# Kernel tuning notes

Measured on AMD Instinct MI355X. Metric: run time of the kernel, lower is better.

## Reference

```python
import jax, jax.numpy as jnp
import numpy as np


def setup_inputs() -> dict:
    key = jax.random.key(0)
    ks = jax.random.split(key, 10)
    B, N, F, H = 4, 512, 64, 4
    x = jax.random.normal(ks[0], (B, N, F), dtype=jnp.float32)
    adj = jax.random.uniform(ks[1], (N, N), dtype=jnp.float32)
    s = 1.0 / np.sqrt(F)
    Wq = jax.random.normal(ks[2], (F, F * H), dtype=jnp.float32) * s
    bq = jnp.zeros((F * H,), dtype=jnp.float32)
    Wk = jax.random.normal(ks[3], (F, F * H), dtype=jnp.float32) * s
    bk = jnp.zeros((F * H,), dtype=jnp.float32)
    Wlin = jax.random.normal(ks[4], (H, F), dtype=jnp.float32) * (1.0 / np.sqrt(H))
    blin = jnp.zeros((F,), dtype=jnp.float32)
    Wfc = jax.random.normal(ks[5], (F, F), dtype=jnp.float32) * s
    bfc = jnp.zeros((F,), dtype=jnp.float32)
    return {"x": x, "adj": adj, "Wq": Wq, "bq": bq, "Wk": Wk, "bk": bk,
            "Wlin": Wlin, "blin": blin, "Wfc": Wfc, "bfc": bfc}


def reference(x, adj, Wq, bq, Wk, bk, Wlin, blin, Wfc, bfc):
    B, N, F = x.shape
    H = Wlin.shape[0]
    # multi-head attention matrix (value projection is computed but unused in the original)
    q = (x @ Wq + bq).reshape(B, N, H, F)  # [B,N,H,F]
    k = (x @ Wk + bk).reshape(B, N, H, F)
    scores = jnp.einsum('bihf,bjhf->bhij', q, k) / jnp.sqrt(jnp.float32(F))
    attn = jax.nn.softmax(scores, axis=-1)  # [B,H,N,N]
    # linear over heads: [B,N,N,H] @ [H,F] -> [B,N,N,F]
    SV2 = jnp.einsum('bhij,hf->bijf', attn, Wlin) + blin
    # symmetric normalization of (adj + I)
    A = adj + jnp.eye(N, dtype=adj.dtype)
    d = jnp.sum(A, axis=1) ** -0.5
    noradj = d[:, None] * A * d[None, :]  # [N,N]
    # sum over dim 1 (source index i) of noradj[i,j]*SV2[b,i,j,f]*x[b,j,f]
    S = jnp.einsum('ij,bijf->bjf', noradj, SV2)
    sx = x * S  # [B,N,F]
    out = jnp.einsum('ij,bjf->bif', noradj, sx)
    out = out @ Wfc + bfc
    return jax.nn.relu(out)
```

## Files before the change

### kernel.cpp

```cpp
#include <hip/hip_runtime.h>
#include <math.h>

#define NN 512
#define FF 64
#define HH 4


__global__ __launch_bounds__(256) void k_s1(const float* __restrict__ x,
                                            const float* __restrict__ Wq,
                                            const float* __restrict__ bq,
                                            const float* __restrict__ Wk,
                                            const float* __restrict__ bk,
                                            const float* __restrict__ adj,
                                            float* __restrict__ q_t,
                                            float* __restrict__ kT,
                                            float* __restrict__ dinv,
                                            float* __restrict__ T,
                                            float* __restrict__ cvec) {
    __shared__ float x_lds[4][64];
    int blk = blockIdx.x, tid = threadIdx.x;
    int wave = tid >> 6, lane = tid & 63;

    if (blk < 512 && wave == 0) {
        float acc = 0.f;
#pragma unroll
        for (int k = 0; k < 8; ++k) acc += adj[(long)blk * NN + k * 64 + lane];
        for (int o = 32; o > 0; o >>= 1) acc += __shfl_xor(acc, o);
        if (lane == 0) dinv[blk] = 1.0f / sqrtf(acc + 1.0f);
    }
    if (blk < 128 && wave == 1) T[blk * 64 + lane] = 0.f;
    if (blk < 8 && wave == 2) cvec[blk * 64 + lane] = 0.f;

    int b = blk >> 8, rest = blk & 255, isK = rest >> 7, itile = rest & 127;
    int i0 = itile * 4;
    x_lds[tid >> 6][tid & 63] = x[((long)b * NN + i0 + (tid >> 6)) * FF + (tid & 63)];
    __syncthreads();
    const float* W = isK ? Wk : Wq;
    float bv = (isK ? bk : bq)[tid];
    float a0 = bv, a1 = bv, a2 = bv, a3 = bv;
    for (int cc = 0; cc < 64; ++cc) {
        float w = W[cc * 256 + tid];
        a0 = fmaf(x_lds[0][cc], w, a0);
        a1 = fmaf(x_lds[1][cc], w, a1);
        a2 = fmaf(x_lds[2][cc], w, a2);
        a3 = fmaf(x_lds[3][cc], w, a3);
    }
    int h = tid >> 6, f = tid & 63;
    int bh = b * HH + h;
    if (!isK) {
        long base = ((long)bh * NN + i0) * FF + f;
        q_t[base] = a0; q_t[base + FF] = a1;
        q_t[base + 2 * FF] = a2; q_t[base + 3 * FF] = a3;
    } else {
        float* kp = kT + (((long)(bh * 16 + (f >> 2)) * NN + i0) << 2) + (f & 3);
        kp[0] = a0; kp[4] = a1; kp[8] = a2; kp[12] = a3;
    }
}

__global__ __launch_bounds__(256) void k_s2(const float* __restrict__ q_t,
                                            const float* __restrict__ kT,
                                            const float* __restrict__ adj,
                                            const float* __restrict__ dinv,
                                            float* __restrict__ T,
                                            float* __restrict__ cvec) {
    __shared__ float q_lds[8][64];
    __shared__ float red[8][4];
    __shared__ float red2[8][4];
    int blk = blockIdx.x, tid = threadIdx.x;
    int itile = blk & 63, h = (blk >> 6) & 3, b = blk >> 8;
    int bh = b * HH + h, i0 = itile * 8;
    int wv = tid >> 6, lane = tid & 63;
#pragma unroll
    for (int k = 0; k < 2; ++k) {
        int idx = k * 256 + tid;
        q_lds[idx >> 6][idx & 63] =
            q_t[((long)bh * NN + i0 + (idx >> 6)) * FF + (idx & 63)];
    }
    __syncthreads();
    int j0 = tid, j1 = tid + 256;
    const float4* kb4 = (const float4*)kT + (long)bh * 16 * NN;
    float s0[8], s1[8];
#pragma unroll
    for (int r = 0; r < 8; ++r) { s0[r] = 0.f; s1[r] = 0.f; }
#pragma unroll 4
    for (int g = 0; g < 16; ++g) {
        float4 kv0 = kb4[g * NN + j0];
        float4 kv1 = kb4[g * NN + j1];
#pragma unroll
        for (int r = 0; r < 8; ++r) {
            float4 qv = *(const float4*)&q_lds[r][g * 4];
            s0[r] = fmaf(qv.x, kv0.x, s0[r]);
            s0[r] = fmaf(qv.y, kv0.y, s0[r]);
            s0[r] = fmaf(qv.z, kv0.z, s0[r]);
            s0[r] = fmaf(qv.w, kv0.w, s0[r]);
            s1[r] = fmaf(qv.x, kv1.x, s1[r]);
            s1[r] = fmaf(qv.y, kv1.y, s1[r]);
            s1[r] = fmaf(qv.z, kv1.z, s1[r]);
            s1[r] = fmaf(qv.w, kv1.w, s1[r]);
        }
    }
    const float scale = 0.125f;
    float m[8];
#pragma unroll
    for (int r = 0; r < 8; ++r) {
        float v = fmaxf(s0[r], s1[r]);
        for (int o = 32; o > 0; o >>= 1) v = fmaxf(v, __shfl_xor(v, o));
        if (lane == 0) red[r][wv] = v;
    }
    __syncthreads();
#pragma unroll
    for (int r = 0; r < 8; ++r)
        m[r] = fmaxf(fmaxf(red[r][0], red[r][1]), fmaxf(red[r][2], red[r][3]));
#pragma unroll
    for (int r = 0; r < 8; ++r) {
        s0[r] = __expf((s0[r] - m[r]) * scale);
        s1[r] = __expf((s1[r] - m[r]) * scale);
        float v = s0[r] + s1[r];
        for (int o = 32; o > 0; o >>= 1) v += __shfl_xor(v, o);
        if (lane == 0) red2[r][wv] = v;
    }
    __syncthreads();
    float dj0 = dinv[j0], dj1 = dinv[j1];
    float pw0 = 0.f, pw1 = 0.f, cw0 = 0.f, cw1 = 0.f;
#pragma unroll
    for (int r = 0; r < 8; ++r) {
        float Zi = 1.0f / (red2[r][0] + red2[r][1] + red2[r][2] + red2[r][3]);
        int gi = i0 + r;
        float di = dinv[gi];
        float a0 = adj[(long)gi * NN + j0] + (gi == j0 ? 1.f : 0.f);
        float a1 = adj[(long)gi * NN + j1] + (gi == j1 ? 1.f : 0.f);
        float t0 = di * a0, t1 = di * a1;
        pw0 = fmaf(t0, s0[r] * Zi, pw0);
        pw1 = fmaf(t1, s1[r] * Zi, pw1);
        cw0 += t0;
        cw1 += t1;
    }
    atomicAdd(&T[bh * NN + j0], pw0 * dj0);
    atomicAdd(&T[bh * NN + j1], pw1 * dj1);
    if (b == 0 && h == 0) {
        atomicAdd(&cvec[j0], cw0);
        atomicAdd(&cvec[j1], cw1);
    }
}

__global__ __launch_bounds__(256) void k_s3(const float* __restrict__ x,
                                            const float* __restrict__ T,
                                            const float* __restrict__ Wlin,
                                            const float* __restrict__ blin,
                                            const float* __restrict__ cvec,
                                            const float* __restrict__ adj,
                                            const float* __restrict__ dinv,
                                            const float* __restrict__ Wfc,
                                            const float* __restrict__ bfc,
                                            float* __restrict__ out) {
    __shared__ float4 u4_l[NN];
    __shared__ float  u0_l[NN];
    __shared__ float2 ad_l[NN];
    __shared__ float part[4][2][64];
    __shared__ float m_lds[2][64];
    __shared__ float part2[4][2][64];
    int blk = blockIdx.x, tid = threadIdx.x;
    int b = blk >> 8, itile = blk & 255;
    int i0 = itile * 2;

    for (int jj = tid; jj < NN; jj += 256) {
        float dj = dinv[jj];
        u0_l[jj] = dj * dj * cvec[jj];
        u4_l[jj] = make_float4(dj * T[(b * HH + 0) * NN + jj],
                               dj * T[(b * HH + 1) * NN + jj],
                               dj * T[(b * HH + 2) * NN + jj],
                               dj * T[(b * HH + 3) * NN + jj]);
        ad_l[jj] = make_float2(adj[(long)i0 * NN + jj] + (i0 == jj ? 1.f : 0.f),
                               adj[(long)(i0 + 1) * NN + jj] + (i0 + 1 == jj ? 1.f : 0.f));
    }
    __syncthreads();

    int f = tid & 63, jc = tid >> 6;
    int jb = jc * 128;
    float blf = blin[f];
    float4 wl = make_float4(Wlin[f], Wlin[64 + f], Wlin[128 + f], Wlin[192 + f]);
    const float* xb = x + (long)b * NN * FF + f;
    float a0 = 0.f, a1 = 0.f;
#pragma unroll 4
    for (int j = jb; j < jb + 128; ++j) {
        float xv = xb[(long)j * FF];
        float4 u = u4_l[j];
        float2 ad = ad_l[j];
        float S = blf * u0_l[j];
        S = fmaf(wl.x, u.x, S);
        S = fmaf(wl.y, u.y, S);
        S = fmaf(wl.z, u.z, S);
        S = fmaf(wl.w, u.w, S);
        float sx = xv * S;
        a0 = fmaf(ad.x, sx, a0);
        a1 = fmaf(ad.y, sx, a1);
    }
    part[jc][0][f] = a0;
    part[jc][1][f] = a1;
    __syncthreads();
    if (jc == 0) {
        m_lds[0][f] = (part[0][0][f] + part[1][0][f] + part[2][0][f] + part[3][0][f]) * dinv[i0];
        m_lds[1][f] = (part[0][1][f] + part[1][1][f] + part[2][1][f] + part[3][1][f]) * dinv[i0 + 1];
    }
    __syncthreads();
    float o0 = 0.f, o1 = 0.f;
    int c0 = jc * 16;
#pragma unroll
    for (int cc = 0; cc < 16; ++cc) {
        float w = Wfc[(c0 + cc) * FF + f];
        o0 = fmaf(m_lds[0][c0 + cc], w, o0);
        o1 = fmaf(m_lds[1][c0 + cc], w, o1);
    }
    part2[jc][0][f] = o0;
    part2[jc][1][f] = o1;
    __syncthreads();
    if (jc == 0) {
        float bb = bfc[f];
        float r0 = part2[0][0][f] + part2[1][0][f] + part2[2][0][f] + part2[3][0][f] + bb;
        float r1 = part2[0][1][f] + part2[1][1][f] + part2[2][1][f] + part2[3][1][f] + bb;
        out[((long)b * NN + i0) * FF + f]     = fmaxf(r0, 0.f);
        out[((long)b * NN + i0 + 1) * FF + f] = fmaxf(r1, 0.f);
    }
}

extern "C" void kernel_launch(void* const* d_in, const int* in_sizes, int n_in,
                              void* d_out, int out_size, void* d_ws, size_t ws_size,
                              hipStream_t stream) {
    const float* x    = (const float*)d_in[0];
    const float* adj  = (const float*)d_in[1];
    const float* Wq   = (const float*)d_in[2];
    const float* bq   = (const float*)d_in[3];
    const float* Wk   = (const float*)d_in[4];
    const float* bk   = (const float*)d_in[5];
    const float* Wlin = (const float*)d_in[6];
    const float* blin = (const float*)d_in[7];
    const float* Wfc  = (const float*)d_in[8];
    const float* bfc  = (const float*)d_in[9];
    float* out = (float*)d_out;

    float* ws   = (float*)d_ws;
    float* dinv = ws;
    float* cvec = ws + 512;
    float* T    = ws + 1024;
    float* q_t  = ws + 9216;
    float* kT   = ws + 2106368;

    k_s1<<<dim3(1024), dim3(256), 0, stream>>>(x, Wq, bq, Wk, bk, adj, q_t, kT, dinv, T, cvec);
    k_s2<<<dim3(1024), dim3(256), 0, stream>>>(q_t, kT, adj, dinv, T, cvec);
    k_s3<<<dim3(1024), dim3(256), 0, stream>>>(x, T, Wlin, blin, cvec, adj, dinv, Wfc, bfc, out);
}
```

Measured before the change: 110.2 us.

## Restructure attention and aggregation kernels for per-wave rows and larger output tiles

The score kernel now gives each wave two query rows across all 512 keys, so the softmax max and sum reductions stay inside a wave. Column contributions are combined through LDS before one atomic per column, replacing per-thread atomics and block-wide syncs. The final kernel handles 8 output rows per 512-thread block, reusing each x load and S computation across 8 rows, and the first kernel reads x as a transposed float4. In exchange there is more LDS per block and fewer, larger blocks in the last stage, which may lower occupancy.

```diff
diff --git a/kernel.cpp b/kernel.cpp
--- a/kernel.cpp
+++ b/kernel.cpp
@@ -17,7 +17,7 @@
                                             float* __restrict__ dinv,
                                             float* __restrict__ T,
                                             float* __restrict__ cvec) {
-    __shared__ float x_lds[4][64];
+    __shared__ float xT[64][4];
     int blk = blockIdx.x, tid = threadIdx.x;
     int wave = tid >> 6, lane = tid & 63;
 
@@ -33,17 +33,22 @@
 
     int b = blk >> 8, rest = blk & 255, isK = rest >> 7, itile = rest & 127;
     int i0 = itile * 4;
-    x_lds[tid >> 6][tid & 63] = x[((long)b * NN + i0 + (tid >> 6)) * FF + (tid & 63)];
+    {
+        int r = tid >> 6, c = tid & 63;
+        xT[c][r] = x[((long)b * NN + i0 + r) * FF + c];
+    }
     __syncthreads();
     const float* W = isK ? Wk : Wq;
     float bv = (isK ? bk : bq)[tid];
     float a0 = bv, a1 = bv, a2 = bv, a3 = bv;
+#pragma unroll 8
     for (int cc = 0; cc < 64; ++cc) {
+        float4 xr = *(const float4*)&xT[cc][0];
         float w = W[cc * 256 + tid];
-        a0 = fmaf(x_lds[0][cc], w, a0);
-        a1 = fmaf(x_lds[1][cc], w, a1);
-        a2 = fmaf(x_lds[2][cc], w, a2);
-        a3 = fmaf(x_lds[3][cc], w, a3);
+        a0 = fmaf(xr.x, w, a0);
+        a1 = fmaf(xr.y, w, a1);
+        a2 = fmaf(xr.z, w, a2);
+        a3 = fmaf(xr.w, w, a3);
     }
     int h = tid >> 6, f = tid & 63;
     int bh = b * HH + h;
@@ -63,87 +68,89 @@
                                             const float* __restrict__ dinv,
                                             float* __restrict__ T,
                                             float* __restrict__ cvec) {
-    __shared__ float q_lds[8][64];
-    __shared__ float red[8][4];
-    __shared__ float red2[8][4];
+    __shared__ float ql[8][64];
+    __shared__ float pwl[4][NN];
+    __shared__ float cwl[4][NN];
     int blk = blockIdx.x, tid = threadIdx.x;
-    int itile = blk & 63, h = (blk >> 6) & 3, b = blk >> 8;
-    int bh = b * HH + h, i0 = itile * 8;
+    int bh = blk >> 6, itile = blk & 63;
+    int i0 = itile * 8;
     int wv = tid >> 6, lane = tid & 63;
+
 #pragma unroll
     for (int k = 0; k < 2; ++k) {
         int idx = k * 256 + tid;
-        q_lds[idx >> 6][idx & 63] =
+        ql[idx >> 6][idx & 63] =
             q_t[((long)bh * NN + i0 + (idx >> 6)) * FF + (idx & 63)];
     }
     __syncthreads();
-    int j0 = tid, j1 = tid + 256;
+
+    int r0 = 2 * wv;
     const float4* kb4 = (const float4*)kT + (long)bh * 16 * NN;
     float s0[8], s1[8];
 #pragma unroll
-    for (int r = 0; r < 8; ++r) { s0[r] = 0.f; s1[r] = 0.f; }
-#pragma unroll 4
+    for (int c = 0; c < 8; ++c) { s0[c] = 0.f; s1[c] = 0.f; }
+#pragma unroll 2
     for (int g = 0; g < 16; ++g) {
-        float4 kv0 = kb4[g * NN + j0];
-        float4 kv1 = kb4[g * NN + j1];
-#pragma unroll
-        for (int r = 0; r < 8; ++r) {
-            float4 qv = *(const float4*)&q_lds[r][g * 4];
-            s0[r] = fmaf(qv.x, kv0.x, s0[r]);
-            s0[r] = fmaf(qv.y, kv0.y, s0[r]);
-            s0[r] = fmaf(qv.z, kv0.z, s0[r]);
-            s0[r] = fmaf(qv.w, kv0.w, s0[r]);
-            s1[r] = fmaf(qv.x, kv1.x, s1[r]);
-            s1[r] = fmaf(qv.y, kv1.y, s1[r]);
-            s1[r] = fmaf(qv.z, kv1.z, s1[r]);
-            s1[r] = fmaf(qv.w, kv1.w, s1[r]);
+        float4 q0 = *(const float4*)&ql[r0][g * 4];
+        float4 q1 = *(const float4*)&ql[r0 + 1][g * 4];
+#pragma unroll
+        for (int c = 0; c < 8; ++c) {
+            float4 kv = kb4[g * NN + c * 64 + lane];
+            s0[c] = fmaf(q0.x, kv.x, s0[c]);
+            s0[c] = fmaf(q0.y, kv.y, s0[c]);
+            s0[c] = fmaf(q0.z, kv.z, s0[c]);
+            s0[c] = fmaf(q0.w, kv.w, s0[c]);
+            s1[c] = fmaf(q1.x, kv.x, s1[c]);
+            s1[c] = fmaf(q1.y, kv.y, s1[c]);
+            s1[c] = fmaf(q1.z, kv.z, s1[c]);
+            s1[c] = fmaf(q1.w, kv.w, s1[c]);
         }
     }
     const float scale = 0.125f;
-    float m[8];
-#pragma unroll
-    for (int r = 0; r < 8; ++r) {
-        float v = fmaxf(s0[r], s1[r]);
-        for (int o = 32; o > 0; o >>= 1) v = fmaxf(v, __shfl_xor(v, o));
-        if (lane == 0) red[r][wv] = v;
-    }
-    __syncthreads();
-#pragma unroll
-    for (int r = 0; r < 8; ++r)
-        m[r] = fmaxf(fmaxf(red[r][0], red[r][1]), fmaxf(red[r][2], red[r][3]));
-#pragma unroll
-    for (int r = 0; r < 8; ++r) {
-        s0[r] = __expf((s0[r] - m[r]) * scale);
-        s1[r] = __expf((s1[r] - m[r]) * scale);
-        float v = s0[r] + s1[r];
-        for (int o = 32; o > 0; o >>= 1) v += __shfl_xor(v, o);
-        if (lane == 0) red2[r][wv] = v;
-    }
-    __syncthreads();
-    float dj0 = dinv[j0], dj1 = dinv[j1];
-    float pw0 = 0.f, pw1 = 0.f, cw0 = 0.f, cw1 = 0.f;
-#pragma unroll
-    for (int r = 0; r < 8; ++r) {
-        float Zi = 1.0f / (red2[r][0] + red2[r][1] + red2[r][2] + red2[r][3]);
-        int gi = i0 + r;
-        float di = dinv[gi];
-        float a0 = adj[(long)gi * NN + j0] + (gi == j0 ? 1.f : 0.f);
-        float a1 = adj[(long)gi * NN + j1] + (gi == j1 ? 1.f : 0.f);
-        float t0 = di * a0, t1 = di * a1;
-        pw0 = fmaf(t0, s0[r] * Zi, pw0);
-        pw1 = fmaf(t1, s1[r] * Zi, pw1);
-        cw0 += t0;
-        cw1 += t1;
-    }
-    atomicAdd(&T[bh * NN + j0], pw0 * dj0);
-    atomicAdd(&T[bh * NN + j1], pw1 * dj1);
-    if (b == 0 && h == 0) {
-        atomicAdd(&cvec[j0], cw0);
-        atomicAdd(&cvec[j1], cw1);
-    }
-}
-
-__global__ __launch_bounds__(256) void k_s3(const float* __restrict__ x,
+    float m0 = s0[0], m1 = s1[0];
+#pragma unroll
+    for (int c = 1; c < 8; ++c) { m0 = fmaxf(m0, s0[c]); m1 = fmaxf(m1, s1[c]); }
+    for (int o = 32; o > 0; o >>= 1) {
+        m0 = fmaxf(m0, __shfl_xor(m0, o));
+        m1 = fmaxf(m1, __shfl_xor(m1, o));
+    }
+    float z0 = 0.f, z1 = 0.f;
+#pragma unroll
+    for (int c = 0; c < 8; ++c) {
+        s0[c] = __expf((s0[c] - m0) * scale);
+        s1[c] = __expf((s1[c] - m1) * scale);
+        z0 += s0[c]; z1 += s1[c];
+    }
+    for (int o = 32; o > 0; o >>= 1) {
+        z0 += __shfl_xor(z0, o);
+        z1 += __shfl_xor(z1, o);
+    }
+    float Zi0 = 1.0f / z0, Zi1 = 1.0f / z1;
+    int gi0 = i0 + r0, gi1 = gi0 + 1;
+    float d0 = dinv[gi0] * Zi0, d1 = dinv[gi1] * Zi1;
+    float e0 = dinv[gi0], e1 = dinv[gi1];
+#pragma unroll
+    for (int c = 0; c < 8; ++c) {
+        int j = c * 64 + lane;
+        float a0 = adj[(long)gi0 * NN + j] + (gi0 == j ? 1.f : 0.f);
+        float a1 = adj[(long)gi1 * NN + j] + (gi1 == j ? 1.f : 0.f);
+        pwl[wv][j] = fmaf(d0 * a0, s0[c], d1 * a1 * s1[c]);
+        cwl[wv][j] = fmaf(e0, a0, e1 * a1);
+    }
+    __syncthreads();
+#pragma unroll
+    for (int k = 0; k < 2; ++k) {
+        int j = k * 256 + tid;
+        float v = pwl[0][j] + pwl[1][j] + pwl[2][j] + pwl[3][j];
+        atomicAdd(&T[bh * NN + j], v * dinv[j]);
+        if (bh == 0) {
+            float w = cwl[0][j] + cwl[1][j] + cwl[2][j] + cwl[3][j];
+            atomicAdd(&cvec[j], w);
+        }
+    }
+}
+
+__global__ __launch_bounds__(512) void k_s3(const float* __restrict__ x,
                                             const float* __restrict__ T,
                                             const float* __restrict__ Wlin,
                                             const float* __restrict__ blin,
@@ -155,71 +162,77 @@
                                             float* __restrict__ out) {
     __shared__ float4 u4_l[NN];
     __shared__ float  u0_l[NN];
-    __shared__ float2 ad_l[NN];
-    __shared__ float part[4][2][64];
-    __shared__ float m_lds[2][64];
-    __shared__ float part2[4][2][64];
+    __shared__ float  adt[NN][8];
+    __shared__ float  part[8][8][64];
+    __shared__ float  m_lds[8][64];
     int blk = blockIdx.x, tid = threadIdx.x;
-    int b = blk >> 8, itile = blk & 255;
-    int i0 = itile * 2;
-
-    for (int jj = tid; jj < NN; jj += 256) {
+    int b = blk >> 6, itile = blk & 63;
+    int i0 = itile * 8;
+
+    {
+        int jj = tid;
         float dj = dinv[jj];
         u0_l[jj] = dj * dj * cvec[jj];
-        u4_l[jj] = make_float4(dj * T[(b * HH + 0) * NN + jj],
-                               dj * T[(b * HH + 1) * NN + jj],
-                               dj * T[(b * HH + 2) * NN + jj],
-                               dj * T[(b * HH + 3) * NN + jj]);
-        ad_l[jj] = make_float2(adj[(long)i0 * NN + jj] + (i0 == jj ? 1.f : 0.f),
-                               adj[(long)(i0 + 1) * NN + jj] + (i0 + 1 == jj ? 1.f : 0.f));
+        const float* Tb = T + (long)b * HH * NN;
+        u4_l[jj] = make_float4(dj * Tb[jj], dj * Tb[NN + jj],
+                               dj * Tb[2 * NN + jj], dj * Tb[3 * NN + jj]);
+        float av[8];
+#pragma unroll
+        for (int r = 0; r < 8; ++r)
+            av[r] = adj[(long)(i0 + r) * NN + jj] + (i0 + r == jj ? 1.f : 0.f);
+        *(float4*)&adt[jj][0] = make_float4(av[0], av[1], av[2], av[3]);
+        *(float4*)&adt[jj][4] = make_float4(av[4], av[5], av[6], av[7]);
     }
     __syncthreads();
 
     int f = tid & 63, jc = tid >> 6;
-    int jb = jc * 128;
+    int jb = jc * 64;
     float blf = blin[f];
     float4 wl = make_float4(Wlin[f], Wlin[64 + f], Wlin[128 + f], Wlin[192 + f]);
     const float* xb = x + (long)b * NN * FF + f;
-    float a0 = 0.f, a1 = 0.f;
+    float a[8];
+#pragma unroll
+    for (int r = 0; r < 8; ++r) a[r] = 0.f;
 #pragma unroll 4
-    for (int j = jb; j < jb + 128; ++j) {
+    for (int j = jb; j < jb + 64; ++j) {
         float xv = xb[(long)j * FF];
         float4 u = u4_l[j];
-        float2 ad = ad_l[j];
         float S = blf * u0_l[j];
         S = fmaf(wl.x, u.x, S);
         S = fmaf(wl.y, u.y, S);
         S = fmaf(wl.z, u.z, S);
         S = fmaf(wl.w, u.w, S);
         float sx = xv * S;
-        a0 = fmaf(ad.x, sx, a0);
-        a1 = fmaf(ad.y, sx, a1);
-    }
-    part[jc][0][f] = a0;
-    part[jc][1][f] = a1;
-    __syncthreads();
-    if (jc == 0) {
-        m_lds[0][f] = (part[0][0][f] + part[1][0][f] + part[2][0][f] + part[3][0][f]) * dinv[i0];
-        m_lds[1][f] = (part[0][1][f] + part[1][1][f] + part[2][1][f] + part[3][1][f]) * dinv[i0 + 1];
-    }
-    __syncthreads();
-    float o0 = 0.f, o1 = 0.f;
-    int c0 = jc * 16;
-#pragma unroll
-    for (int cc = 0; cc < 16; ++cc) {
-        float w = Wfc[(c0 + cc) * FF + f];
-        o0 = fmaf(m_lds[0][c0 + cc], w, o0);
-        o1 = fmaf(m_lds[1][c0 + cc], w, o1);
-    }
-    part2[jc][0][f] = o0;
-    part2[jc][1][f] = o1;
-    __syncthreads();
-    if (jc == 0) {
-        float bb = bfc[f];
-        float r0 = part2[0][0][f] + part2[1][0][f] + part2[2][0][f] + part2[3][0][f] + bb;
-        float r1 = part2[0][1][f] + part2[1][1][f] + part2[2][1][f] + part2[3][1][f] + bb;
-        out[((long)b * NN + i0) * FF + f]     = fmaxf(r0, 0.f);
-        out[((long)b * NN + i0 + 1) * FF + f] = fmaxf(r1, 0.f);
+        float4 t0 = *(const float4*)&adt[j][0];
+        float4 t1 = *(const float4*)&adt[j][4];
+        a[0] = fmaf(t0.x, sx, a[0]);
+        a[1] = fmaf(t0.y, sx, a[1]);
+        a[2] = fmaf(t0.z, sx, a[2]);
+        a[3] = fmaf(t0.w, sx, a[3]);
+        a[4] = fmaf(t1.x, sx, a[4]);
+        a[5] = fmaf(t1.y, sx, a[5]);
+        a[6] = fmaf(t1.z, sx, a[6]);
+        a[7] = fmaf(t1.w, sx, a[7]);
+    }
+#pragma unroll
+    for (int r = 0; r < 8; ++r) part[jc][r][f] = a[r];
+    __syncthreads();
+
+    {
+        int r = tid >> 6;
+        float s = 0.f;
+#pragma unroll
+        for (int c = 0; c < 8; ++c) s += part[c][r][f];
+        m_lds[r][f] = s * dinv[i0 + r];
+    }
+    __syncthreads();
+    {
+        int r = tid >> 6;
+        float o = bfc[f];
+#pragma unroll 8
+        for (int cc = 0; cc < 64; ++cc)
+            o = fmaf(m_lds[r][cc], Wfc[cc * FF + f], o);
+        out[((long)b * NN + i0 + r) * FF + f] = fmaxf(o, 0.f);
     }
 }
 
@@ -247,5 +260,5 @@
 
     k_s1<<<dim3(1024), dim3(256), 0, stream>>>(x, Wq, bq, Wk, bk, adj, q_t, kT, dinv, T, cvec);
     k_s2<<<dim3(1024), dim3(256), 0, stream>>>(q_t, kT, adj, dinv, T, cvec);
-    k_s3<<<dim3(1024), dim3(256), 0, stream>>>(x, T, Wlin, blin, cvec, adj, dinv, Wfc, bfc, out);
-}
+    k_s3<<<dim3(256), dim3(512), 0, stream>>>(x, T, Wlin, blin, cvec, adj, dinv, Wfc, bfc, out);
+}
```

Measured after the change: 108.6 us. About the same (-1.5%).
